# Performance work log

Measured on AMD Instinct MI355X. Metric: run time of the kernel, lower is better.

Reference implementation:

```python
import jax, jax.numpy as jnp
import numpy as np

# Module hyperparameters (from init_kwargs)
K = 1.0                       # init_curvature (registered buffer, non-trainable)
HOPFIELD_DIM = 64
BETA = 1.0 / np.sqrt(float(HOPFIELD_DIM))  # beta=None default -> 1/sqrt(d_h)
EPS = 1e-7

# ---- Lorentz / hyperboloid ops (geoopt conventions, curvature param k>0) ----

def _to_tangent0(x):
    # x: (..., d) Euclidean -> (..., d+1) in T_0 H via [0, x], norm-clipped to 3.5
    zeros = jnp.zeros(x.shape[:-1] + (1,), x.dtype)
    x = jnp.concatenate([zeros, x], axis=-1)
    n = jnp.linalg.norm(x, axis=-1, keepdims=True)
    factor = jnp.minimum(3.5 / (n + 1e-7), 1.0)
    return x * factor

def expmap0(x_euc):
    # (..., d) Euclidean -> (..., d+1) on hyperboloid via Exp_0([0, x])
    u = _to_tangent0(x_euc)
    x = u[..., 1:]
    sqrtk = jnp.sqrt(K)
    xn = jnp.maximum(jnp.linalg.norm(x, axis=-1, keepdims=True), EPS)
    theta = xn / sqrtk
    return jnp.concatenate(
        [sqrtk * jnp.cosh(theta), sqrtk * jnp.sinh(theta) * x / xn], axis=-1)

def logmap0(y):
    # (..., d+1) on hyperboloid -> (..., d) tangent at origin (spatial part)
    sqrtk = jnp.sqrt(K)
    y0 = y[..., :1]
    yr = y[..., 1:]
    yn = jnp.maximum(jnp.linalg.norm(yr, axis=-1, keepdims=True), EPS)
    d = sqrtk * jnp.arccosh(jnp.maximum(y0 / sqrtk, 1.0 + EPS))
    return d * yr / yn

def minkowski_inner(u, v):
    # <u,v>_L = -u0 v0 + sum_i u_i v_i ; returns (...) without last dim
    return -u[..., 0] * v[..., 0] + jnp.sum(u[..., 1:] * v[..., 1:], axis=-1)

# ---- KFCore forward ----

def _kfcore(queries, keys, values, Wq, bq, Wk, bk, Wv, bv):
    sqrtk = jnp.sqrt(K)
    Qe = queries @ Wq.T + bq                     # (B,S,d_h)
    Ke = keys @ Wk.T + bk                        # (B,M,d_h)
    Ve = (values @ Wk.T + bk) @ Wv.T + bv        # (B,M,d_out)
    Q = expmap0(Qe)                              # (B,S,d+1)
    Kh = expmap0(Ke)                             # (B,M,d+1)
    V = expmap0(Ve)                              # (B,M,d+1)

    dp1 = Q.shape[-1]
    sign = jnp.concatenate([-jnp.ones((1,), Q.dtype), jnp.ones((dp1 - 1,), Q.dtype)])

    # Minkowski inner pairwise: (B,S,M)
    sims = jnp.einsum('bsd,bmd->bsm', Q * sign, Kh)
    alpha = jax.nn.softmax(-BETA * sims, axis=-1)          # (B,S,M)

    # Karcher flow: tangent_mean = sum_m alpha * logmap_Q(V_m)
    # logmap_x(y) = dist(x,y) * (y + (<x,y>/k) x) / ||y + (<x,y>/k) x||_L
    ip = jnp.einsum('bsd,bmd->bsm', Q * sign, V)           # <Q_s, V_m>_L
    dist = sqrtk * jnp.arccosh(jnp.maximum(-ip / K, 1.0 + EPS))
    qq = minkowski_inner(Q, Q)[:, :, None]                 # (B,S,1)
    vv = minkowski_inner(V, V)[:, None, :]                 # (B,1,M)
    c = ip / K
    nomin_sq = vv + 2.0 * c * ip + c * c * qq              # ||nomin||_L^2, (B,S,M)
    denom = jnp.sqrt(jnp.maximum(nomin_sq, EPS))
    w = alpha * dist / denom                               # (B,S,M)
    # sum_m w * (V_m + c * Q_s)  -- avoids the (B,S,M,d+1) logmap tensor
    tm = jnp.einsum('bsm,bmd->bsd', w, V) \
         + jnp.sum(w * c, axis=-1, keepdims=True) * Q      # (B,S,d+1)

    # expmap_Q(tm) = cosh(||tm||/sqrtk) Q + sqrtk sinh(||tm||/sqrtk) tm/||tm||
    un = jnp.sqrt(jnp.maximum(minkowski_inner(tm, tm), EPS))[..., None]
    th = un / sqrtk
    z = jnp.cosh(th) * Q + sqrtk * jnp.sinh(th) * tm / un
    return logmap0(z)                                      # (B,S,d_out)


def setup_inputs() -> dict:
    key = jax.random.key(0)
    ks = jax.random.split(key, 9)
    B, S, M = 2, 2048, 4096
    SD, MD, DH, DO = 256, 256, 64, 64
    sq = 1.0 / np.sqrt(SD)
    sm = 1.0 / np.sqrt(MD)
    sh = 1.0 / np.sqrt(DH)
    return {
        'queries': jax.random.normal(ks[0], (B, S, SD), jnp.float32),
        'keys':    jax.random.normal(ks[1], (B, M, MD), jnp.float32),
        'values':  jax.random.normal(ks[2], (B, M, MD), jnp.float32),
        'Wq': jax.random.normal(ks[3], (DH, SD), jnp.float32) * sq,
        'bq': jax.random.normal(ks[4], (DH,), jnp.float32) * sq,
        'Wk': jax.random.normal(ks[5], (DH, MD), jnp.float32) * sm,
        'bk': jax.random.normal(ks[6], (DH,), jnp.float32) * sm,
        'Wv': jax.random.normal(ks[7], (DO, DH), jnp.float32) * sh,
        'bv': jax.random.normal(ks[8], (DO,), jnp.float32) * sh,
    }


def reference(queries, keys, values, Wq, bq, Wk, bk, Wv, bv):
    return _kfcore(queries, keys, values, Wq, bq, Wk, bk, Wv, bv)
```

## Files before the change

### kernel.cpp

```cpp
#include <hip/hip_runtime.h>
#include <math.h>

#define BETA  0.125f
#define SHIFT 30.0f
#define EPSF  1e-7f

typedef __attribute__((ext_vector_type(8))) short short8;
typedef __attribute__((ext_vector_type(4))) short short4v;
typedef __attribute__((ext_vector_type(4))) float f32x4;

__device__ __forceinline__ unsigned short bf16_rne(float x) {
  unsigned int u = __float_as_uint(x);
  return (unsigned short)((u + 0x7fffu + ((u >> 16) & 1u)) >> 16);
}
__device__ __forceinline__ float bf16_tof(unsigned short h) {
  return __uint_as_float(((unsigned int)h) << 16);
}
__device__ __forceinline__ void split2(float x, unsigned short& h, unsigned short& l) {
  unsigned int u = __float_as_uint(x);
  unsigned int hr = (u + 0x7fffu + ((u >> 16) & 1u)) & 0xffff0000u;
  h = (unsigned short)(hr >> 16);
  l = bf16_rne(x - __uint_as_float(hr));
}

__global__ __launch_bounds__(256) void proj_kernel(
    const float* __restrict__ Xq, const float* __restrict__ Xk,
    const float* __restrict__ Xv,
    const float* __restrict__ Wq, const float* __restrict__ bq,
    const float* __restrict__ Wk, const float* __restrict__ bk,
    const float* __restrict__ Wv, const float* __restrict__ bv,
    float* __restrict__ Q0, float* __restrict__ K0, float* __restrict__ V0,
    unsigned short* __restrict__ Qh, unsigned short* __restrict__ Ql,
    unsigned short* __restrict__ Kh, unsigned short* __restrict__ Kl,
    unsigned short* __restrict__ Vh, unsigned short* __restrict__ Vl,
    unsigned short* __restrict__ Vth, unsigned short* __restrict__ Vtl)
{
  __shared__ float Xs[64 * 64];
  __shared__ float Ws[64 * 64];
  __shared__ unsigned int Tr[64 * 65];

  const int bid = blockIdx.x;
  const float *X, *W, *bias;
  float* y0;
  unsigned short *yh, *yl;
  bool dbl;
  int rowBase;
  if (bid < 64)       { X = Xq; W = Wq; bias = bq; y0 = Q0; yh = Qh; yl = Ql; rowBase = bid << 6;         dbl = false; }
  else if (bid < 192) { X = Xk; W = Wk; bias = bk; y0 = K0; yh = Kh; yl = Kl; rowBase = (bid - 64) << 6;  dbl = false; }
  else                { X = Xv; W = Wk; bias = bk; y0 = V0; yh = Vh; yl = Vl; rowBase = (bid - 192) << 6; dbl = true;  }

  const int tid = threadIdx.x;
  const int ty = tid >> 4, tx = tid & 15;
  const int ty4 = ty << 2, tx4 = tx << 2;

  float acc[4][4];
#pragma unroll
  for (int j = 0; j < 4; ++j) {
    float bj = bias[tx4 + j];
#pragma unroll
    for (int i = 0; i < 4; ++i) acc[i][j] = bj;
  }

  for (int kc = 0; kc < 4; ++kc) {
#pragma unroll
    for (int q = 0; q < 4; ++q) {
      int f = tid + (q << 8);
      int r = f >> 4, g = f & 15;
      int sw = (r << 6) + ((g ^ (r >> 2)) << 2);
      *(float4*)&Xs[sw] = *(const float4*)&X[(rowBase + r) * 256 + (kc << 6) + (g << 2)];
      *(float4*)&Ws[sw] = *(const float4*)&W[r * 256 + (kc << 6) + (g << 2)];
    }
    __syncthreads();
#pragma unroll 4
    for (int kk = 0; kk < 64; kk += 4) {
      const int gk = kk >> 2;
      float4 xa[4], wb[4];
#pragma unroll
      for (int i = 0; i < 4; ++i)
        xa[i] = *(const float4*)&Xs[((ty4 + i) << 6) + ((gk ^ ty) << 2)];
#pragma unroll
      for (int j = 0; j < 4; ++j)
        wb[j] = *(const float4*)&Ws[((tx4 + j) << 6) + ((gk ^ tx) << 2)];
#pragma unroll
      for (int i = 0; i < 4; ++i)
#pragma unroll
        for (int j = 0; j < 4; ++j)
          acc[i][j] += xa[i].x * wb[j].x + xa[i].y * wb[j].y +
                       xa[i].z * wb[j].z + xa[i].w * wb[j].w;
    }
    __syncthreads();
  }

  if (dbl) {
#pragma unroll
    for (int i = 0; i < 4; ++i) {
      float4 v = make_float4(acc[i][0], acc[i][1], acc[i][2], acc[i][3]);
      *(float4*)&Xs[((ty4 + i) << 6) + ((tx ^ ty) << 2)] = v;
    }
#pragma unroll
    for (int q = 0; q < 4; ++q) {
      int f = tid + (q << 8);
      int r = f >> 4, g = f & 15;
      int sw = (r << 6) + ((g ^ (r >> 2)) << 2);
      *(float4*)&Ws[sw] = *(const float4*)&Wv[(r << 6) + (g << 2)];
    }
#pragma unroll
    for (int j = 0; j < 4; ++j) {
      float bj = bv[tx4 + j];
#pragma unroll
      for (int i = 0; i < 4; ++i) acc[i][j] = bj;
    }
    __syncthreads();
#pragma unroll 4
    for (int kk = 0; kk < 64; kk += 4) {
      const int gk = kk >> 2;
      float4 xa[4], wb[4];
#pragma unroll
      for (int i = 0; i < 4; ++i)
        xa[i] = *(const float4*)&Xs[((ty4 + i) << 6) + ((gk ^ ty) << 2)];
#pragma unroll
      for (int j = 0; j < 4; ++j)
        wb[j] = *(const float4*)&Ws[((tx4 + j) << 6) + ((gk ^ tx) << 2)];
#pragma unroll
      for (int i = 0; i < 4; ++i)
#pragma unroll
        for (int j = 0; j < 4; ++j)
          acc[i][j] += xa[i].x * wb[j].x + xa[i].y * wb[j].y +
                       xa[i].z * wb[j].z + xa[i].w * wb[j].w;
    }
  }

  float n2p[4];
#pragma unroll
  for (int i = 0; i < 4; ++i)
    n2p[i] = acc[i][0] * acc[i][0] + acc[i][1] * acc[i][1] +
             acc[i][2] * acc[i][2] + acc[i][3] * acc[i][3];
#pragma unroll
  for (int i = 0; i < 4; ++i) {
    n2p[i] += __shfl_xor(n2p[i], 1);
    n2p[i] += __shfl_xor(n2p[i], 2);
    n2p[i] += __shfl_xor(n2p[i], 4);
    n2p[i] += __shfl_xor(n2p[i], 8);
  }
  unsigned short hv[4][4], lv[4][4];
#pragma unroll
  for (int i = 0; i < 4; ++i) {
    float n = sqrtf(n2p[i]);
    float factor = fminf(3.5f / (n + EPSF), 1.0f);
    float xn = fmaxf(n * factor, EPSF);
    float et = __expf(xn);
    float rt = __builtin_amdgcn_rcpf(et);
    float ch = 0.5f * (et + rt);
    float sh = 0.5f * (et - rt);
    float scale = sh * factor * __builtin_amdgcn_rcpf(xn);
    int row = rowBase + ty4 + i;
    if (tx == 0) y0[row] = ch;
#pragma unroll
    for (int j = 0; j < 4; ++j) split2(acc[i][j] * scale, hv[i][j], lv[i][j]);
    unsigned int* ph = (unsigned int*)(yh + row * 64 + tx4);
    ph[0] = (unsigned int)hv[i][0] | ((unsigned int)hv[i][1] << 16);
    ph[1] = (unsigned int)hv[i][2] | ((unsigned int)hv[i][3] << 16);
    unsigned int* pl = (unsigned int*)(yl + row * 64 + tx4);
    pl[0] = (unsigned int)lv[i][0] | ((unsigned int)lv[i][1] << 16);
    pl[1] = (unsigned int)lv[i][2] | ((unsigned int)lv[i][3] << 16);
  }

  if (dbl) {
#pragma unroll
    for (int i = 0; i < 4; ++i)
#pragma unroll
      for (int j = 0; j < 4; ++j)
        Tr[(ty4 + i) * 65 + tx4 + j] = (unsigned int)hv[i][j];
    __syncthreads();
#pragma unroll
    for (int q = 0; q < 2; ++q) {
      int f = tid + (q << 8);
      int d = f >> 3;
      int seg = (f & 7) << 3;
      unsigned int o[4];
#pragma unroll
      for (int k = 0; k < 4; ++k)
        o[k] = Tr[(seg + 2 * k) * 65 + d] | (Tr[(seg + 2 * k + 1) * 65 + d] << 16);
      *(uint4*)&Vth[d * 8192 + rowBase + seg] = make_uint4(o[0], o[1], o[2], o[3]);
    }
    __syncthreads();
#pragma unroll
    for (int i = 0; i < 4; ++i)
#pragma unroll
      for (int j = 0; j < 4; ++j)
        Tr[(ty4 + i) * 65 + tx4 + j] = (unsigned int)lv[i][j];
    __syncthreads();
#pragma unroll
    for (int q = 0; q < 2; ++q) {
      int f = tid + (q << 8);
      int d = f >> 3;
      int seg = (f & 7) << 3;
      unsigned int o[4];
#pragma unroll
      for (int k = 0; k < 4; ++k)
        o[k] = Tr[(seg + 2 * k) * 65 + d] | (Tr[(seg + 2 * k + 1) * 65 + d] << 16);
      *(uint4*)&Vtl[d * 8192 + rowBase + seg] = make_uint4(o[0], o[1], o[2], o[3]);
    }
  }
}

__global__ void __attribute__((amdgpu_waves_per_eu(2, 2)))
__launch_bounds__(256) attn_kernel(
    const float* __restrict__ Q0g, const unsigned short* __restrict__ Qh,
    const unsigned short* __restrict__ Ql,
    const float* __restrict__ K0g, const unsigned short* __restrict__ Kh,
    const unsigned short* __restrict__ Kl,
    const float* __restrict__ V0g, const unsigned short* __restrict__ Vh,
    const unsigned short* __restrict__ Vl,
    const unsigned short* __restrict__ Vth, const unsigned short* __restrict__ Vtl,
    float* __restrict__ Tpart, float* __restrict__ T0part,
    float* __restrict__ Lpart, float* __restrict__ WCpart,
    int SL, int nChunk)
{
  __shared__ unsigned short Wlds[4 * 32 * 68];

  const int tid = threadIdx.x;
  const int wave = tid >> 6, lane = tid & 63;
  const int lm = lane & 15;
  const int lg = lane >> 4;
  const int Wid = blockIdx.x * 4 + wave;
  const int slice = Wid % SL;
  const int sT = (Wid / SL) & 63;
  const int b = Wid / (SL * 64);
  const int sBase = b * 2048 + sT * 32;

  unsigned short* wbase = Wlds + wave * (32 * 68);

  short8 qf[2][2][2];
#pragma unroll
  for (int si = 0; si < 2; ++si)
#pragma unroll
    for (int ks = 0; ks < 2; ++ks) {
      int idx = (sBase + si * 16 + lm) * 64 + ks * 32 + lg * 8;
      qf[si][ks][0] = *(const short8*)(Qh + idx);
      qf[si][ks][1] = *(const short8*)(Ql + idx);
    }
  float q0r[2][4];
#pragma unroll
  for (int si = 0; si < 2; ++si)
#pragma unroll
    for (int r = 0; r < 4; ++r)
      q0r[si][r] = Q0g[sBase + si * 16 + lg * 4 + r];

  f32x4 accT[2][4];
  float Lp[2][4], WCp[2][4], T0p[2][4];
#pragma unroll
  for (int si = 0; si < 2; ++si)
#pragma unroll
    for (int r = 0; r < 4; ++r) {
      Lp[si][r] = 0.f; WCp[si][r] = 0.f; T0p[si][r] = 0.f;
    }
#pragma unroll
  for (int si = 0; si < 2; ++si)
#pragma unroll
    for (int dj = 0; dj < 4; ++dj) accT[si][dj] = f32x4{0.f, 0.f, 0.f, 0.f};

  const int mSliceBase = b * 4096 + slice * (nChunk * 64);
  for (int mc = 0; mc < nChunk; ++mc) {
    const int mCh = mSliceBase + (mc << 6);
    float k0r[4], v0r[4];
#pragma unroll
    for (int mj = 0; mj < 4; ++mj) {
      k0r[mj] = K0g[mCh + mj * 16 + lm];
      v0r[mj] = V0g[mCh + mj * 16 + lm];
    }

    f32x4 sims[2][4], ipv[2][4];
#pragma unroll
    for (int si = 0; si < 2; ++si)
#pragma unroll
      for (int mj = 0; mj < 4; ++mj) {
        sims[si][mj] = f32x4{0.f, 0.f, 0.f, 0.f};
        ipv[si][mj]  = f32x4{0.f, 0.f, 0.f, 0.f};
      }
#pragma unroll
    for (int mj = 0; mj < 4; ++mj) {
#pragma unroll
      for (int ks = 0; ks < 2; ++ks) {
        int bidx = (mCh + mj * 16 + lm) * 64 + ks * 32 + lg * 8;
        short8 kh = *(const short8*)(Kh + bidx);
        short8 kl = *(const short8*)(Kl + bidx);
        short8 vh = *(const short8*)(Vh + bidx);
        short8 vl = *(const short8*)(Vl + bidx);
#pragma unroll
        for (int si = 0; si < 2; ++si) {
          sims[si][mj] = __builtin_amdgcn_mfma_f32_16x16x32_bf16(qf[si][ks][0], kh, sims[si][mj], 0, 0, 0);
          sims[si][mj] = __builtin_amdgcn_mfma_f32_16x16x32_bf16(qf[si][ks][0], kl, sims[si][mj], 0, 0, 0);
          sims[si][mj] = __builtin_amdgcn_mfma_f32_16x16x32_bf16(qf[si][ks][1], kh, sims[si][mj], 0, 0, 0);
          ipv[si][mj]  = __builtin_amdgcn_mfma_f32_16x16x32_bf16(qf[si][ks][0], vh, ipv[si][mj], 0, 0, 0);
          ipv[si][mj]  = __builtin_amdgcn_mfma_f32_16x16x32_bf16(qf[si][ks][0], vl, ipv[si][mj], 0, 0, 0);
          ipv[si][mj]  = __builtin_amdgcn_mfma_f32_16x16x32_bf16(qf[si][ks][1], vh, ipv[si][mj], 0, 0, 0);
        }
      }
    }

#pragma unroll
    for (int si = 0; si < 2; ++si)
#pragma unroll
      for (int mj = 0; mj < 4; ++mj)
#pragma unroll
        for (int r = 0; r < 4; ++r) {
          float c  = ipv[si][mj][r]  - q0r[si][r] * v0r[mj];
          float sm = sims[si][mj][r] - q0r[si][r] * k0r[mj];
          float x = -c;
          float s2 = fmaxf(fmaf(x, x, -1.0f), EPSF);
          float rs = __builtin_amdgcn_rsqf(s2);
          float dist = __logf(fmaf(s2, rs, x));
          float e = __expf(fmaf(-BETA, sm, -SHIFT));
          float w = e * dist * rs;
          unsigned short wu = bf16_rne(w);
          float wb = bf16_tof(wu);
          Lp[si][r]  += e;
          WCp[si][r] += wb * c;
          T0p[si][r] += wb * v0r[mj];
          wbase[(si * 16 + lg * 4 + r) * 68 + mj * 16 + lm] = wu;
        }

#pragma unroll
    for (int ks = 0; ks < 2; ++ks) {
      short8 wa[2];
#pragma unroll
      for (int si = 0; si < 2; ++si) {
        const unsigned short* p = wbase + (si * 16 + lm) * 68 + ks * 32 + lg * 8;
        short4v a0 = *(const short4v*)p;
        short4v a1 = *(const short4v*)(p + 4);
        wa[si] = __builtin_shufflevector(a0, a1, 0, 1, 2, 3, 4, 5, 6, 7);
      }
#pragma unroll
      for (int dj = 0; dj < 4; ++dj) {
        int vidx = (dj * 16 + lm) * 8192 + mCh + ks * 32 + lg * 8;
        short8 th = *(const short8*)(Vth + vidx);
        short8 tl = *(const short8*)(Vtl + vidx);
#pragma unroll
        for (int si = 0; si < 2; ++si) {
          accT[si][dj] = __builtin_amdgcn_mfma_f32_16x16x32_bf16(wa[si], th, accT[si][dj], 0, 0, 0);
          accT[si][dj] = __builtin_amdgcn_mfma_f32_16x16x32_bf16(wa[si], tl, accT[si][dj], 0, 0, 0);
        }
      }
    }
  }

#pragma unroll
  for (int si = 0; si < 2; ++si)
#pragma unroll
    for (int r = 0; r < 4; ++r)
#pragma unroll
      for (int off = 1; off < 16; off <<= 1) {
        Lp[si][r]  += __shfl_xor(Lp[si][r], off);
        WCp[si][r] += __shfl_xor(WCp[si][r], off);
        T0p[si][r] += __shfl_xor(T0p[si][r], off);
      }

  const int rowP = (slice << 12) + sBase;
#pragma unroll
  for (int si = 0; si < 2; ++si)
#pragma unroll
    for (int r = 0; r < 4; ++r) {
      int row = rowP + si * 16 + lg * 4 + r;
#pragma unroll
      for (int dj = 0; dj < 4; ++dj)
        Tpart[row * 64 + dj * 16 + lm] = accT[si][dj][r];
      if (lm == 0) {
        Lpart[row]  = Lp[si][r];
        WCpart[row] = WCp[si][r];
        T0part[row] = T0p[si][r];
      }
    }
}

__global__ __launch_bounds__(256) void combine_kernel(
    const float* __restrict__ Q0, const unsigned short* __restrict__ Qh,
    const unsigned short* __restrict__ Ql,
    const float* __restrict__ Tpart, const float* __restrict__ T0part,
    const float* __restrict__ Lpart, const float* __restrict__ WCpart,
    float* __restrict__ out, int nSl)
{
  int wid = (blockIdx.x << 2) + (threadIdx.x >> 6);
  int lane = threadIdx.x & 63;

  float Tsum = 0.f, T0 = 0.f, L = 0.f, WC = 0.f;
#pragma unroll 4
  for (int sli = 0; sli < nSl; ++sli) {
    int rp = (sli << 12) + wid;
    Tsum += Tpart[rp * 64 + lane];
    T0 += T0part[rp];
    L  += Lpart[rp];
    WC += WCpart[rp];
  }
  int qi = wid * 64 + lane;
  float qd = bf16_tof(Qh[qi]) + bf16_tof(Ql[qi]);
  float q0 = Q0[wid];
  float invL = 1.0f / L;
  float td = Tsum * invL;
  float t0 = T0 * invL;
  float wc = WC * invL;

  double tt = (double)td * (double)td;
#pragma unroll
  for (int off = 1; off < 64; off <<= 1) tt += __shfl_xor(tt, off);
  tt -= (double)t0 * (double)t0;
  double mk = tt + (double)wc * (double)wc;

  float un = (float)sqrt(fmax(mk, 1e-12));
  float eu = __expf(un);
  float ru = 1.0f / eu;
  float ch = 0.5f * (eu + ru);
  float shu = 0.5f * (eu - ru) / un;

  float tmd = td + wc * qd;
  float tm0 = t0 + wc * q0;
  float zd = ch * qd + shu * tmd;
  float z0 = ch * q0 + shu * tm0;

  float p2 = zd * zd;
#pragma unroll
  for (int off = 1; off < 64; off <<= 1) p2 += __shfl_xor(p2, off);
  float yn = fmaxf(sqrtf(p2), EPSF);
  float zc = fmaxf(z0, 1.0f + EPSF);
  float dl = __logf(zc + sqrtf(fmaxf(zc * zc - 1.0f, 0.f)));
  out[qi] = dl * zd / yn;
}

extern "C" void kernel_launch(void* const* d_in, const int* in_sizes, int n_in,
                              void* d_out, int out_size, void* d_ws, size_t ws_size,
                              hipStream_t stream)
{
  const float* queries = (const float*)d_in[0];
  const float* keys    = (const float*)d_in[1];
  const float* values  = (const float*)d_in[2];
  const float* Wq      = (const float*)d_in[3];
  const float* bq      = (const float*)d_in[4];
  const float* Wk      = (const float*)d_in[5];
  const float* bk      = (const float*)d_in[6];
  const float* Wv      = (const float*)d_in[7];
  const float* bv      = (const float*)d_in[8];
  float* out = (float*)d_out;
  float* ws  = (float*)d_ws;

  const size_t base = 1855488;
  auto need = [&](size_t sl) {
    return (base + sl * 4096 * 64 + 3 * sl * 4096) * 4;
  };
  int SL = 16;
  if (ws_size < need(16)) SL = 8;
  const int nChunk = 4096 / (SL * 64);

  float* Q0 = ws;
  float* K0 = ws + 4096;
  float* V0 = ws + 12288;
  unsigned short* Qh  = (unsigned short*)(ws + 20480);
  unsigned short* Ql  = (unsigned short*)(ws + 151552);
  unsigned short* Kh  = (unsigned short*)(ws + 282624);
  unsigned short* Kl  = (unsigned short*)(ws + 544768);
  unsigned short* Vh  = (unsigned short*)(ws + 806912);
  unsigned short* Vl  = (unsigned short*)(ws + 1069056);
  unsigned short* Vth = (unsigned short*)(ws + 1331200);
  unsigned short* Vtl = (unsigned short*)(ws + 1593344);
  float* Tpart  = ws + base;
  float* T0part = Tpart + (size_t)SL * 4096 * 64;
  float* Lpart  = T0part + (size_t)SL * 4096;
  float* WCpart = Lpart + (size_t)SL * 4096;

  proj_kernel<<<320, 256, 0, stream>>>(queries, keys, values, Wq, bq, Wk, bk,
                                       Wv, bv, Q0, K0, V0, Qh, Ql, Kh, Kl,
                                       Vh, Vl, Vth, Vtl);
  attn_kernel<<<32 * SL, 256, 0, stream>>>(
      Q0, Qh, Ql, K0, Kh, Kl, V0, Vh, Vl, Vth, Vtl,
      Tpart, T0part, Lpart, WCpart, SL, nChunk);
  combine_kernel<<<1024, 256, 0, stream>>>(
      Q0, Qh, Ql, Tpart, T0part, Lpart, WCpart, out, SL);
}
```

Measured before the change: 163.8 us.

## Shrink attention tiles to 16 rows and reduce slice partials with float atomics

Each attention wave now handles 16 query rows instead of 32, and the launch grows to 1024 blocks with a fixed 16-way split over M. Partial results go through float atomics into one zeroed accumulator, which proj_kernel clears, instead of per-slice partial buffers that combine_kernel had to sum. The launch bound changes to allow more occupancy, and proj block order is reshuffled so V is projected first. The risk is halving the reuse of each K/V fragment per MFMA, atomic contention, and a summation order that is no longer deterministic.

```diff
diff --git a/kernel.cpp b/kernel.cpp
--- a/kernel.cpp
+++ b/kernel.cpp
@@ -22,6 +22,8 @@
   h = (unsigned short)(hr >> 16);
   l = bf16_rne(x - __uint_as_float(hr));
 }
+
+#define ZERO_F4 68608
 
 __global__ __launch_bounds__(256) void proj_kernel(
     const float* __restrict__ Xq, const float* __restrict__ Xk,
@@ -33,23 +35,31 @@
     unsigned short* __restrict__ Qh, unsigned short* __restrict__ Ql,
     unsigned short* __restrict__ Kh, unsigned short* __restrict__ Kl,
     unsigned short* __restrict__ Vh, unsigned short* __restrict__ Vl,
-    unsigned short* __restrict__ Vth, unsigned short* __restrict__ Vtl)
+    unsigned short* __restrict__ Vth, unsigned short* __restrict__ Vtl,
+    float* __restrict__ zeroRegion)
 {
   __shared__ float Xs[64 * 64];
   __shared__ float Ws[64 * 64];
   __shared__ unsigned int Tr[64 * 65];
 
   const int bid = blockIdx.x;
+  const int tid = threadIdx.x;
+
+  {
+    int idx = bid * 256 + tid;
+    if (idx < ZERO_F4)
+      *(float4*)&zeroRegion[idx * 4] = make_float4(0.f, 0.f, 0.f, 0.f);
+  }
+
   const float *X, *W, *bias;
   float* y0;
   unsigned short *yh, *yl;
   bool dbl;
   int rowBase;
-  if (bid < 64)       { X = Xq; W = Wq; bias = bq; y0 = Q0; yh = Qh; yl = Ql; rowBase = bid << 6;         dbl = false; }
-  else if (bid < 192) { X = Xk; W = Wk; bias = bk; y0 = K0; yh = Kh; yl = Kl; rowBase = (bid - 64) << 6;  dbl = false; }
-  else                { X = Xv; W = Wk; bias = bk; y0 = V0; yh = Vh; yl = Vl; rowBase = (bid - 192) << 6; dbl = true;  }
-
-  const int tid = threadIdx.x;
+  if (bid < 128)      { X = Xv; W = Wk; bias = bk; y0 = V0; yh = Vh; yl = Vl; rowBase = bid << 6;         dbl = true;  }
+  else if (bid < 256) { X = Xk; W = Wk; bias = bk; y0 = K0; yh = Kh; yl = Kl; rowBase = (bid - 128) << 6; dbl = false; }
+  else                { X = Xq; W = Wq; bias = bq; y0 = Q0; yh = Qh; yl = Ql; rowBase = (bid - 256) << 6; dbl = false; }
+
   const int ty = tid >> 4, tx = tid & 15;
   const int ty4 = ty << 2, tx4 = tx << 2;
 
@@ -204,8 +214,7 @@
   }
 }
 
-__global__ void __attribute__((amdgpu_waves_per_eu(2, 2)))
-__launch_bounds__(256) attn_kernel(
+__global__ __launch_bounds__(256, 4) void attn_kernel(
     const float* __restrict__ Q0g, const unsigned short* __restrict__ Qh,
     const unsigned short* __restrict__ Ql,
     const float* __restrict__ K0g, const unsigned short* __restrict__ Kh,
@@ -213,55 +222,44 @@
     const float* __restrict__ V0g, const unsigned short* __restrict__ Vh,
     const unsigned short* __restrict__ Vl,
     const unsigned short* __restrict__ Vth, const unsigned short* __restrict__ Vtl,
-    float* __restrict__ Tpart, float* __restrict__ T0part,
-    float* __restrict__ Lpart, float* __restrict__ WCpart,
-    int SL, int nChunk)
+    float* __restrict__ Tacc, float* __restrict__ T0acc,
+    float* __restrict__ Lacc, float* __restrict__ WCacc)
 {
-  __shared__ unsigned short Wlds[4 * 32 * 68];
+  __shared__ unsigned short Wlds[4 * 16 * 68];
 
   const int tid = threadIdx.x;
   const int wave = tid >> 6, lane = tid & 63;
   const int lm = lane & 15;
   const int lg = lane >> 4;
   const int Wid = blockIdx.x * 4 + wave;
-  const int slice = Wid % SL;
-  const int sT = (Wid / SL) & 63;
-  const int b = Wid / (SL * 64);
-  const int sBase = b * 2048 + sT * 32;
-
-  unsigned short* wbase = Wlds + wave * (32 * 68);
-
-  short8 qf[2][2][2];
-#pragma unroll
-  for (int si = 0; si < 2; ++si)
-#pragma unroll
-    for (int ks = 0; ks < 2; ++ks) {
-      int idx = (sBase + si * 16 + lm) * 64 + ks * 32 + lg * 8;
-      qf[si][ks][0] = *(const short8*)(Qh + idx);
-      qf[si][ks][1] = *(const short8*)(Ql + idx);
-    }
-  float q0r[2][4];
-#pragma unroll
-  for (int si = 0; si < 2; ++si)
-#pragma unroll
-    for (int r = 0; r < 4; ++r)
-      q0r[si][r] = Q0g[sBase + si * 16 + lg * 4 + r];
-
-  f32x4 accT[2][4];
-  float Lp[2][4], WCp[2][4], T0p[2][4];
-#pragma unroll
-  for (int si = 0; si < 2; ++si)
-#pragma unroll
-    for (int r = 0; r < 4; ++r) {
-      Lp[si][r] = 0.f; WCp[si][r] = 0.f; T0p[si][r] = 0.f;
-    }
-#pragma unroll
-  for (int si = 0; si < 2; ++si)
-#pragma unroll
-    for (int dj = 0; dj < 4; ++dj) accT[si][dj] = f32x4{0.f, 0.f, 0.f, 0.f};
-
-  const int mSliceBase = b * 4096 + slice * (nChunk * 64);
-  for (int mc = 0; mc < nChunk; ++mc) {
+  const int slice = Wid & 15;
+  const int sTb = Wid >> 4;
+  const int sT = sTb & 127;
+  const int b = sTb >> 7;
+  const int sBase = b * 2048 + sT * 16;
+
+  unsigned short* wbase = Wlds + wave * (16 * 68);
+
+  short8 qf[2][2];
+#pragma unroll
+  for (int ks = 0; ks < 2; ++ks) {
+    int idx = (sBase + lm) * 64 + ks * 32 + lg * 8;
+    qf[ks][0] = *(const short8*)(Qh + idx);
+    qf[ks][1] = *(const short8*)(Ql + idx);
+  }
+  float q0r[4];
+#pragma unroll
+  for (int r = 0; r < 4; ++r) q0r[r] = Q0g[sBase + lg * 4 + r];
+
+  f32x4 accT[4];
+  float Lp[4], WCp[4], T0p[4];
+#pragma unroll
+  for (int r = 0; r < 4; ++r) { Lp[r] = 0.f; WCp[r] = 0.f; T0p[r] = 0.f; }
+#pragma unroll
+  for (int dj = 0; dj < 4; ++dj) accT[dj] = f32x4{0.f, 0.f, 0.f, 0.f};
+
+  const int mSliceBase = b * 4096 + slice * 256;
+  for (int mc = 0; mc < 4; ++mc) {
     const int mCh = mSliceBase + (mc << 6);
     float k0r[4], v0r[4];
 #pragma unroll
@@ -270,14 +268,12 @@
       v0r[mj] = V0g[mCh + mj * 16 + lm];
     }
 
-    f32x4 sims[2][4], ipv[2][4];
-#pragma unroll
-    for (int si = 0; si < 2; ++si)
-#pragma unroll
-      for (int mj = 0; mj < 4; ++mj) {
-        sims[si][mj] = f32x4{0.f, 0.f, 0.f, 0.f};
-        ipv[si][mj]  = f32x4{0.f, 0.f, 0.f, 0.f};
-      }
+    f32x4 sims[4], ipv[4];
+#pragma unroll
+    for (int mj = 0; mj < 4; ++mj) {
+      sims[mj] = f32x4{0.f, 0.f, 0.f, 0.f};
+      ipv[mj]  = f32x4{0.f, 0.f, 0.f, 0.f};
+    }
 #pragma unroll
     for (int mj = 0; mj < 4; ++mj) {
 #pragma unroll
@@ -287,112 +283,91 @@
         short8 kl = *(const short8*)(Kl + bidx);
         short8 vh = *(const short8*)(Vh + bidx);
         short8 vl = *(const short8*)(Vl + bidx);
-#pragma unroll
-        for (int si = 0; si < 2; ++si) {
-          sims[si][mj] = __builtin_amdgcn_mfma_f32_16x16x32_bf16(qf[si][ks][0], kh, sims[si][mj], 0, 0, 0);
-          sims[si][mj] = __builtin_amdgcn_mfma_f32_16x16x32_bf16(qf[si][ks][0], kl, sims[si][mj], 0, 0, 0);
-          sims[si][mj] = __builtin_amdgcn_mfma_f32_16x16x32_bf16(qf[si][ks][1], kh, sims[si][mj], 0, 0, 0);
-          ipv[si][mj]  = __builtin_amdgcn_mfma_f32_16x16x32_bf16(qf[si][ks][0], vh, ipv[si][mj], 0, 0, 0);
-          ipv[si][mj]  = __builtin_amdgcn_mfma_f32_16x16x32_bf16(qf[si][ks][0], vl, ipv[si][mj], 0, 0, 0);
-          ipv[si][mj]  = __builtin_amdgcn_mfma_f32_16x16x32_bf16(qf[si][ks][1], vh, ipv[si][mj], 0, 0, 0);
-        }
+        sims[mj] = __builtin_amdgcn_mfma_f32_16x16x32_bf16(qf[ks][0], kh, sims[mj], 0, 0, 0);
+        sims[mj] = __builtin_amdgcn_mfma_f32_16x16x32_bf16(qf[ks][0], kl, sims[mj], 0, 0, 0);
+        sims[mj] = __builtin_amdgcn_mfma_f32_16x16x32_bf16(qf[ks][1], kh, sims[mj], 0, 0, 0);
+        ipv[mj]  = __builtin_amdgcn_mfma_f32_16x16x32_bf16(qf[ks][0], vh, ipv[mj], 0, 0, 0);
+        ipv[mj]  = __builtin_amdgcn_mfma_f32_16x16x32_bf16(qf[ks][0], vl, ipv[mj], 0, 0, 0);
+        ipv[mj]  = __builtin_amdgcn_mfma_f32_16x16x32_bf16(qf[ks][1], vh, ipv[mj], 0, 0, 0);
       }
     }
 
 #pragma unroll
-    for (int si = 0; si < 2; ++si)
-#pragma unroll
-      for (int mj = 0; mj < 4; ++mj)
-#pragma unroll
-        for (int r = 0; r < 4; ++r) {
-          float c  = ipv[si][mj][r]  - q0r[si][r] * v0r[mj];
-          float sm = sims[si][mj][r] - q0r[si][r] * k0r[mj];
-          float x = -c;
-          float s2 = fmaxf(fmaf(x, x, -1.0f), EPSF);
-          float rs = __builtin_amdgcn_rsqf(s2);
-          float dist = __logf(fmaf(s2, rs, x));
-          float e = __expf(fmaf(-BETA, sm, -SHIFT));
-          float w = e * dist * rs;
-          unsigned short wu = bf16_rne(w);
-          float wb = bf16_tof(wu);
-          Lp[si][r]  += e;
-          WCp[si][r] += wb * c;
-          T0p[si][r] += wb * v0r[mj];
-          wbase[(si * 16 + lg * 4 + r) * 68 + mj * 16 + lm] = wu;
-        }
+    for (int mj = 0; mj < 4; ++mj)
+#pragma unroll
+      for (int r = 0; r < 4; ++r) {
+        float c  = ipv[mj][r]  - q0r[r] * v0r[mj];
+        float sm = sims[mj][r] - q0r[r] * k0r[mj];
+        float x = -c;
+        float s2 = fmaxf(fmaf(x, x, -1.0f), EPSF);
+        float rs = __builtin_amdgcn_rsqf(s2);
+        float dist = __logf(fmaf(s2, rs, x));
+        float e = __expf(fmaf(-BETA, sm, -SHIFT));
+        float w = e * dist * rs;
+        unsigned short wu = bf16_rne(w);
+        float wb = bf16_tof(wu);
+        Lp[r]  += e;
+        WCp[r] += wb * c;
+        T0p[r] += wb * v0r[mj];
+        wbase[(lg * 4 + r) * 68 + mj * 16 + lm] = wu;
+      }
 
 #pragma unroll
     for (int ks = 0; ks < 2; ++ks) {
-      short8 wa[2];
-#pragma unroll
-      for (int si = 0; si < 2; ++si) {
-        const unsigned short* p = wbase + (si * 16 + lm) * 68 + ks * 32 + lg * 8;
-        short4v a0 = *(const short4v*)p;
-        short4v a1 = *(const short4v*)(p + 4);
-        wa[si] = __builtin_shufflevector(a0, a1, 0, 1, 2, 3, 4, 5, 6, 7);
-      }
+      const unsigned short* p = wbase + lm * 68 + ks * 32 + lg * 8;
+      short4v a0 = *(const short4v*)p;
+      short4v a1 = *(const short4v*)(p + 4);
+      short8 wa = __builtin_shufflevector(a0, a1, 0, 1, 2, 3, 4, 5, 6, 7);
 #pragma unroll
       for (int dj = 0; dj < 4; ++dj) {
         int vidx = (dj * 16 + lm) * 8192 + mCh + ks * 32 + lg * 8;
         short8 th = *(const short8*)(Vth + vidx);
         short8 tl = *(const short8*)(Vtl + vidx);
-#pragma unroll
-        for (int si = 0; si < 2; ++si) {
-          accT[si][dj] = __builtin_amdgcn_mfma_f32_16x16x32_bf16(wa[si], th, accT[si][dj], 0, 0, 0);
-          accT[si][dj] = __builtin_amdgcn_mfma_f32_16x16x32_bf16(wa[si], tl, accT[si][dj], 0, 0, 0);
-        }
+        accT[dj] = __builtin_amdgcn_mfma_f32_16x16x32_bf16(wa, th, accT[dj], 0, 0, 0);
+        accT[dj] = __builtin_amdgcn_mfma_f32_16x16x32_bf16(wa, tl, accT[dj], 0, 0, 0);
       }
     }
   }
 
 #pragma unroll
-  for (int si = 0; si < 2; ++si)
-#pragma unroll
-    for (int r = 0; r < 4; ++r)
-#pragma unroll
-      for (int off = 1; off < 16; off <<= 1) {
-        Lp[si][r]  += __shfl_xor(Lp[si][r], off);
-        WCp[si][r] += __shfl_xor(WCp[si][r], off);
-        T0p[si][r] += __shfl_xor(T0p[si][r], off);
-      }
-
-  const int rowP = (slice << 12) + sBase;
-#pragma unroll
-  for (int si = 0; si < 2; ++si)
-#pragma unroll
-    for (int r = 0; r < 4; ++r) {
-      int row = rowP + si * 16 + lg * 4 + r;
-#pragma unroll
-      for (int dj = 0; dj < 4; ++dj)
-        Tpart[row * 64 + dj * 16 + lm] = accT[si][dj][r];
-      if (lm == 0) {
-        Lpart[row]  = Lp[si][r];
-        WCpart[row] = WCp[si][r];
-        T0part[row] = T0p[si][r];
-      }
-    }
+  for (int r = 0; r < 4; ++r)
+#pragma unroll
+    for (int off = 1; off < 16; off <<= 1) {
+      Lp[r]  += __shfl_xor(Lp[r], off);
+      WCp[r] += __shfl_xor(WCp[r], off);
+      T0p[r] += __shfl_xor(T0p[r], off);
+    }
+
+#pragma unroll
+  for (int r = 0; r < 4; ++r) {
+    int row = sBase + lg * 4 + r;
+#pragma unroll
+    for (int dj = 0; dj < 4; ++dj)
+      unsafeAtomicAdd(&Tacc[row * 64 + dj * 16 + lm], accT[dj][r]);
+    if (lm == 0) {
+      unsafeAtomicAdd(&Lacc[row],  Lp[r]);
+      unsafeAtomicAdd(&WCacc[row], WCp[r]);
+      unsafeAtomicAdd(&T0acc[row], T0p[r]);
+    }
+  }
 }
 
 __global__ __launch_bounds__(256) void combine_kernel(
     const float* __restrict__ Q0, const unsigned short* __restrict__ Qh,
     const unsigned short* __restrict__ Ql,
-    const float* __restrict__ Tpart, const float* __restrict__ T0part,
-    const float* __restrict__ Lpart, const float* __restrict__ WCpart,
-    float* __restrict__ out, int nSl)
+    const float* __restrict__ Tacc, const float* __restrict__ T0acc,
+    const float* __restrict__ Lacc, const float* __restrict__ WCacc,
+    float* __restrict__ out)
 {
   int wid = (blockIdx.x << 2) + (threadIdx.x >> 6);
   int lane = threadIdx.x & 63;
 
-  float Tsum = 0.f, T0 = 0.f, L = 0.f, WC = 0.f;
-#pragma unroll 4
-  for (int sli = 0; sli < nSl; ++sli) {
-    int rp = (sli << 12) + wid;
-    Tsum += Tpart[rp * 64 + lane];
-    T0 += T0part[rp];
-    L  += Lpart[rp];
-    WC += WCpart[rp];
-  }
   int qi = wid * 64 + lane;
+  float Tsum = Tacc[qi];
+  float T0 = T0acc[wid];
+  float L  = Lacc[wid];
+  float WC = WCacc[wid];
+
   float qd = bf16_tof(Qh[qi]) + bf16_tof(Ql[qi]);
   float q0 = Q0[wid];
   float invL = 1.0f / L;
@@ -442,14 +417,6 @@
   float* out = (float*)d_out;
   float* ws  = (float*)d_ws;
 
-  const size_t base = 1855488;
-  auto need = [&](size_t sl) {
-    return (base + sl * 4096 * 64 + 3 * sl * 4096) * 4;
-  };
-  int SL = 16;
-  if (ws_size < need(16)) SL = 8;
-  const int nChunk = 4096 / (SL * 64);
-
   float* Q0 = ws;
   float* K0 = ws + 4096;
   float* V0 = ws + 12288;
@@ -461,17 +428,17 @@
   unsigned short* Vl  = (unsigned short*)(ws + 1069056);
   unsigned short* Vth = (unsigned short*)(ws + 1331200);
   unsigned short* Vtl = (unsigned short*)(ws + 1593344);
-  float* Tpart  = ws + base;
-  float* T0part = Tpart + (size_t)SL * 4096 * 64;
-  float* Lpart  = T0part + (size_t)SL * 4096;
-  float* WCpart = Lpart + (size_t)SL * 4096;
+  float* Tacc  = ws + 1855488;
+  float* T0acc = ws + 2117632;
+  float* Lacc  = ws + 2121728;
+  float* WCacc = ws + 2125824;
 
   proj_kernel<<<320, 256, 0, stream>>>(queries, keys, values, Wq, bq, Wk, bk,
                                        Wv, bv, Q0, K0, V0, Qh, Ql, Kh, Kl,
-                                       Vh, Vl, Vth, Vtl);
-  attn_kernel<<<32 * SL, 256, 0, stream>>>(
+                                       Vh, Vl, Vth, Vtl, Tacc);
+  attn_kernel<<<1024, 256, 0, stream>>>(
       Q0, Qh, Ql, K0, Kh, Kl, V0, Vh, Vl, Vth, Vtl,
-      Tpart, T0part, Lpart, WCpart, SL, nChunk);
+      Tacc, T0acc, Lacc, WCacc);
   combine_kernel<<<1024, 256, 0, stream>>>(
-      Q0, Qh, Ql, Tpart, T0part, Lpart, WCpart, out, SL);
-}
+      Q0, Qh, Ql, Tacc, T0acc, Lacc, WCacc, out);
+}
```

Measured after the change: 206.4 us. +26.0%, slower.

## Share K/V tiles via LDS across waves and reduce partials with atomics

Applied to the files above, without the earlier changes.

The attention kernel now assigns four waves of a block to different query tiles over the same key slice. The K/V bf16 hi/lo tiles, including the transposed V, are staged once into LDS and reused by all four waves instead of being read from global memory per wave. Per-slice partial outputs are replaced by float atomic adds into a single accumulator, which proj_kernel zero-initialises. This shrinks the combine kernel's read loop, at the cost of extra barriers, atomic contention and non-deterministic summation order.

```diff
diff --git a/kernel.cpp b/kernel.cpp
--- a/kernel.cpp
+++ b/kernel.cpp
@@ -22,6 +22,8 @@
   h = (unsigned short)(hr >> 16);
   l = bf16_rne(x - __uint_as_float(hr));
 }
+
+#define ZERO_F4 68608
 
 __global__ __launch_bounds__(256) void proj_kernel(
     const float* __restrict__ Xq, const float* __restrict__ Xk,
@@ -33,23 +35,31 @@
     unsigned short* __restrict__ Qh, unsigned short* __restrict__ Ql,
     unsigned short* __restrict__ Kh, unsigned short* __restrict__ Kl,
     unsigned short* __restrict__ Vh, unsigned short* __restrict__ Vl,
-    unsigned short* __restrict__ Vth, unsigned short* __restrict__ Vtl)
+    unsigned short* __restrict__ Vth, unsigned short* __restrict__ Vtl,
+    float* __restrict__ zeroRegion)
 {
   __shared__ float Xs[64 * 64];
   __shared__ float Ws[64 * 64];
   __shared__ unsigned int Tr[64 * 65];
 
   const int bid = blockIdx.x;
+  const int tid = threadIdx.x;
+
+  {
+    int idx = bid * 256 + tid;
+    if (idx < ZERO_F4)
+      *(float4*)&zeroRegion[idx * 4] = make_float4(0.f, 0.f, 0.f, 0.f);
+  }
+
   const float *X, *W, *bias;
   float* y0;
   unsigned short *yh, *yl;
   bool dbl;
   int rowBase;
-  if (bid < 64)       { X = Xq; W = Wq; bias = bq; y0 = Q0; yh = Qh; yl = Ql; rowBase = bid << 6;         dbl = false; }
-  else if (bid < 192) { X = Xk; W = Wk; bias = bk; y0 = K0; yh = Kh; yl = Kl; rowBase = (bid - 64) << 6;  dbl = false; }
-  else                { X = Xv; W = Wk; bias = bk; y0 = V0; yh = Vh; yl = Vl; rowBase = (bid - 192) << 6; dbl = true;  }
-
-  const int tid = threadIdx.x;
+  if (bid < 128)      { X = Xv; W = Wk; bias = bk; y0 = V0; yh = Vh; yl = Vl; rowBase = bid << 6;         dbl = true;  }
+  else if (bid < 256) { X = Xk; W = Wk; bias = bk; y0 = K0; yh = Kh; yl = Kl; rowBase = (bid - 128) << 6; dbl = false; }
+  else                { X = Xq; W = Wq; bias = bq; y0 = Q0; yh = Qh; yl = Ql; rowBase = (bid - 256) << 6; dbl = false; }
+
   const int ty = tid >> 4, tx = tid & 15;
   const int ty4 = ty << 2, tx4 = tx << 2;
 
@@ -208,28 +218,28 @@
 __launch_bounds__(256) attn_kernel(
     const float* __restrict__ Q0g, const unsigned short* __restrict__ Qh,
     const unsigned short* __restrict__ Ql,
-    const float* __restrict__ K0g, const unsigned short* __restrict__ Kh,
-    const unsigned short* __restrict__ Kl,
-    const float* __restrict__ V0g, const unsigned short* __restrict__ Vh,
-    const unsigned short* __restrict__ Vl,
-    const unsigned short* __restrict__ Vth, const unsigned short* __restrict__ Vtl,
-    float* __restrict__ Tpart, float* __restrict__ T0part,
-    float* __restrict__ Lpart, float* __restrict__ WCpart,
-    int SL, int nChunk)
+    const float* __restrict__ K0g, const unsigned short* __restrict__ Khg,
+    const unsigned short* __restrict__ Klg,
+    const float* __restrict__ V0g, const unsigned short* __restrict__ Vhg,
+    const unsigned short* __restrict__ Vlg,
+    const unsigned short* __restrict__ Vthg, const unsigned short* __restrict__ Vtlg,
+    float* __restrict__ Tacc, float* __restrict__ T0acc,
+    float* __restrict__ Lacc, float* __restrict__ WCacc)
 {
-  __shared__ unsigned short Wlds[4 * 32 * 68];
+  __shared__ unsigned short LB[6 * 4608];
 
   const int tid = threadIdx.x;
   const int wave = tid >> 6, lane = tid & 63;
   const int lm = lane & 15;
   const int lg = lane >> 4;
-  const int Wid = blockIdx.x * 4 + wave;
-  const int slice = Wid % SL;
-  const int sT = (Wid / SL) & 63;
-  const int b = Wid / (SL * 64);
-  const int sBase = b * 2048 + sT * 32;
-
-  unsigned short* wbase = Wlds + wave * (32 * 68);
+  const int bid = blockIdx.x;
+  const int slice = bid & 15;
+  const int t = bid >> 4;
+  const int b = t >> 4;
+  const int sT = t & 15;
+  const int sBase = b * 2048 + sT * 128 + wave * 32;
+
+  unsigned short* wbase = LB + wave * 2176;
 
   short8 qf[2][2][2];
 #pragma unroll
@@ -260,15 +270,32 @@
 #pragma unroll
     for (int dj = 0; dj < 4; ++dj) accT[si][dj] = f32x4{0.f, 0.f, 0.f, 0.f};
 
-  const int mSliceBase = b * 4096 + slice * (nChunk * 64);
-  for (int mc = 0; mc < nChunk; ++mc) {
+  const int mSliceBase = b * 4096 + slice * 256;
+  const int frow = tid >> 3;
+  const int fc8 = (tid & 7) << 3;
+  for (int mc = 0; mc < 4; ++mc) {
     const int mCh = mSliceBase + (mc << 6);
+
+#pragma unroll
+    for (int q = 0; q < 2; ++q) {
+      int row = frow + (q << 5);
+      int goff = (mCh + row) * 64 + fc8;
+      int loff = row * 72 + fc8;
+      *(uint4*)&LB[loff]            = *(const uint4*)&Khg[goff];
+      *(uint4*)&LB[4608 + loff]     = *(const uint4*)&Klg[goff];
+      *(uint4*)&LB[2 * 4608 + loff] = *(const uint4*)&Vhg[goff];
+      *(uint4*)&LB[3 * 4608 + loff] = *(const uint4*)&Vlg[goff];
+      int gofft = row * 8192 + mCh + fc8;
+      *(uint4*)&LB[4 * 4608 + loff] = *(const uint4*)&Vthg[gofft];
+      *(uint4*)&LB[5 * 4608 + loff] = *(const uint4*)&Vtlg[gofft];
+    }
     float k0r[4], v0r[4];
 #pragma unroll
     for (int mj = 0; mj < 4; ++mj) {
       k0r[mj] = K0g[mCh + mj * 16 + lm];
       v0r[mj] = V0g[mCh + mj * 16 + lm];
     }
+    __syncthreads();
 
     f32x4 sims[2][4], ipv[2][4];
 #pragma unroll
@@ -282,11 +309,11 @@
     for (int mj = 0; mj < 4; ++mj) {
 #pragma unroll
       for (int ks = 0; ks < 2; ++ks) {
-        int bidx = (mCh + mj * 16 + lm) * 64 + ks * 32 + lg * 8;
-        short8 kh = *(const short8*)(Kh + bidx);
-        short8 kl = *(const short8*)(Kl + bidx);
-        short8 vh = *(const short8*)(Vh + bidx);
-        short8 vl = *(const short8*)(Vl + bidx);
+        int off = (mj * 16 + lm) * 72 + ks * 32 + lg * 8;
+        short8 kh = *(const short8*)&LB[off];
+        short8 kl = *(const short8*)&LB[4608 + off];
+        short8 vh = *(const short8*)&LB[2 * 4608 + off];
+        short8 vl = *(const short8*)&LB[3 * 4608 + off];
 #pragma unroll
         for (int si = 0; si < 2; ++si) {
           sims[si][mj] = __builtin_amdgcn_mfma_f32_16x16x32_bf16(qf[si][ks][0], kh, sims[si][mj], 0, 0, 0);
@@ -298,6 +325,7 @@
         }
       }
     }
+    __syncthreads();
 
 #pragma unroll
     for (int si = 0; si < 2; ++si)
@@ -333,9 +361,9 @@
       }
 #pragma unroll
       for (int dj = 0; dj < 4; ++dj) {
-        int vidx = (dj * 16 + lm) * 8192 + mCh + ks * 32 + lg * 8;
-        short8 th = *(const short8*)(Vth + vidx);
-        short8 tl = *(const short8*)(Vtl + vidx);
+        int off = (dj * 16 + lm) * 72 + ks * 32 + lg * 8;
+        short8 th = *(const short8*)&LB[4 * 4608 + off];
+        short8 tl = *(const short8*)&LB[5 * 4608 + off];
 #pragma unroll
         for (int si = 0; si < 2; ++si) {
           accT[si][dj] = __builtin_amdgcn_mfma_f32_16x16x32_bf16(wa[si], th, accT[si][dj], 0, 0, 0);
@@ -343,6 +371,7 @@
         }
       }
     }
+    __syncthreads();
   }
 
 #pragma unroll
@@ -356,19 +385,18 @@
         T0p[si][r] += __shfl_xor(T0p[si][r], off);
       }
 
-  const int rowP = (slice << 12) + sBase;
 #pragma unroll
   for (int si = 0; si < 2; ++si)
 #pragma unroll
     for (int r = 0; r < 4; ++r) {
-      int row = rowP + si * 16 + lg * 4 + r;
+      int row = sBase + si * 16 + lg * 4 + r;
 #pragma unroll
       for (int dj = 0; dj < 4; ++dj)
-        Tpart[row * 64 + dj * 16 + lm] = accT[si][dj][r];
+        unsafeAtomicAdd(&Tacc[row * 64 + dj * 16 + lm], accT[si][dj][r]);
       if (lm == 0) {
-        Lpart[row]  = Lp[si][r];
-        WCpart[row] = WCp[si][r];
-        T0part[row] = T0p[si][r];
+        unsafeAtomicAdd(&Lacc[row],  Lp[si][r]);
+        unsafeAtomicAdd(&WCacc[row], WCp[si][r]);
+        unsafeAtomicAdd(&T0acc[row], T0p[si][r]);
       }
     }
 }
@@ -376,23 +404,19 @@
 __global__ __launch_bounds__(256) void combine_kernel(
     const float* __restrict__ Q0, const unsigned short* __restrict__ Qh,
     const unsigned short* __restrict__ Ql,
-    const float* __restrict__ Tpart, const float* __restrict__ T0part,
-    const float* __restrict__ Lpart, const float* __restrict__ WCpart,
-    float* __restrict__ out, int nSl)
+    const float* __restrict__ Tacc, const float* __restrict__ T0acc,
+    const float* __restrict__ Lacc, const float* __restrict__ WCacc,
+    float* __restrict__ out)
 {
   int wid = (blockIdx.x << 2) + (threadIdx.x >> 6);
   int lane = threadIdx.x & 63;
 
-  float Tsum = 0.f, T0 = 0.f, L = 0.f, WC = 0.f;
-#pragma unroll 4
-  for (int sli = 0; sli < nSl; ++sli) {
-    int rp = (sli << 12) + wid;
-    Tsum += Tpart[rp * 64 + lane];
-    T0 += T0part[rp];
-    L  += Lpart[rp];
-    WC += WCpart[rp];
-  }
   int qi = wid * 64 + lane;
+  float Tsum = Tacc[qi];
+  float T0 = T0acc[wid];
+  float L  = Lacc[wid];
+  float WC = WCacc[wid];
+
   float qd = bf16_tof(Qh[qi]) + bf16_tof(Ql[qi]);
   float q0 = Q0[wid];
   float invL = 1.0f / L;
@@ -442,14 +466,6 @@
   float* out = (float*)d_out;
   float* ws  = (float*)d_ws;
 
-  const size_t base = 1855488;
-  auto need = [&](size_t sl) {
-    return (base + sl * 4096 * 64 + 3 * sl * 4096) * 4;
-  };
-  int SL = 16;
-  if (ws_size < need(16)) SL = 8;
-  const int nChunk = 4096 / (SL * 64);
-
   float* Q0 = ws;
   float* K0 = ws + 4096;
   float* V0 = ws + 12288;
@@ -461,17 +477,17 @@
   unsigned short* Vl  = (unsigned short*)(ws + 1069056);
   unsigned short* Vth = (unsigned short*)(ws + 1331200);
   unsigned short* Vtl = (unsigned short*)(ws + 1593344);
-  float* Tpart  = ws + base;
-  float* T0part = Tpart + (size_t)SL * 4096 * 64;
-  float* Lpart  = T0part + (size_t)SL * 4096;
-  float* WCpart = Lpart + (size_t)SL * 4096;
+  float* Tacc  = ws + 1855488;
+  float* T0acc = ws + 2117632;
+  float* Lacc  = ws + 2121728;
+  float* WCacc = ws + 2125824;
 
   proj_kernel<<<320, 256, 0, stream>>>(queries, keys, values, Wq, bq, Wk, bk,
                                        Wv, bv, Q0, K0, V0, Qh, Ql, Kh, Kl,
-                                       Vh, Vl, Vth, Vtl);
-  attn_kernel<<<32 * SL, 256, 0, stream>>>(
+                                       Vh, Vl, Vth, Vtl, Tacc);
+  attn_kernel<<<512, 256, 0, stream>>>(
       Q0, Qh, Ql, K0, Kh, Kl, V0, Vh, Vl, Vth, Vtl,
-      Tpart, T0part, Lpart, WCpart, SL, nChunk);
+      Tacc, T0acc, Lacc, WCacc);
   combine_kernel<<<1024, 256, 0, stream>>>(
-      Q0, Qh, Ql, Tpart, T0part, Lpart, WCpart, out, SL);
-}
+      Q0, Qh, Ql, Tacc, T0acc, Lacc, WCacc, out);
+}
```

Result: faster. 157.1 us (-4.1%).
